# Kernel optimization log

Hardware: AMD Instinct MI355X
Metric: run time of the kernel (lower is better)

## Reference

```python
import jax, jax.numpy as jnp
import numpy as np

BN_EPS = 1e-5
L2_EPS = 1e-12


def setup_inputs() -> dict:
    key = jax.random.key(0)
    ks = jax.random.split(key, 4)
    B, C, H, W = 16, 384, 56, 56
    x = jax.random.normal(ks[0], (B, C, H, W), dtype=jnp.float32)
    w_qkv = jax.random.normal(ks[1], (3 * C, C), dtype=jnp.float32) * (1.0 / np.sqrt(C))
    b_qkv = jnp.zeros((3 * C,), dtype=jnp.float32)
    w_proj = jax.random.normal(ks[2], (C, C), dtype=jnp.float32) * (1.0 / np.sqrt(C))
    b_proj = jnp.zeros((C,), dtype=jnp.float32)
    bn_gamma = jnp.ones((C,), dtype=jnp.float32)
    bn_beta = jnp.zeros((C,), dtype=jnp.float32)
    bn_mean = jnp.zeros((C,), dtype=jnp.float32)
    bn_var = jnp.ones((C,), dtype=jnp.float32)
    temperature = jnp.ones((1,), dtype=jnp.float32)
    return {"x": x, "w_qkv": w_qkv, "b_qkv": b_qkv, "w_proj": w_proj,
            "b_proj": b_proj, "bn_gamma": bn_gamma, "bn_beta": bn_beta,
            "bn_mean": bn_mean, "bn_var": bn_var, "temperature": temperature}


def _l2norm_lastdim(t):
    # F.normalize(t, dim=-1): divide by max(||t||_2, eps)
    n = jnp.sqrt(jnp.sum(t * t, axis=-1, keepdims=True))
    return t / jnp.maximum(n, L2_EPS)


def reference(x, w_qkv, b_qkv, w_proj, b_proj, bn_gamma, bn_beta, bn_mean, bn_var, temperature):
    B, C, H, W = x.shape
    N = H * W
    # BatchNorm2d (eval mode, running stats)
    scale = bn_gamma / jnp.sqrt(bn_var + BN_EPS)          # [C]
    shift = bn_beta - bn_mean * scale                     # [C]
    xn = x * scale[None, :, None, None] + shift[None, :, None, None]
    # 1x1 conv qkv: C -> 3C, operate on flattened spatial [B, C, N]
    xn_f = xn.reshape(B, C, N)
    qkv = jnp.einsum('oc,bcn->bon', w_qkv, xn_f) + b_qkv[None, :, None]  # [B,3C,N]
    q, k, v = qkv[:, :C], qkv[:, C:2 * C], qkv[:, 2 * C:]
    q = _l2norm_lastdim(q)                                # [B,C,N]
    k = _l2norm_lastdim(k)
    # channel-transposed attention: [B,C,C]
    logits = jnp.einsum('bcn,bdn->bcd', q, k) * temperature[0]
    attn = jax.nn.softmax(logits, axis=-1)
    fused = jnp.einsum('bcd,bdn->bcn', attn, v)           # [B,C,N]
    # 1x1 proj conv + residual
    out = jnp.einsum('oc,bcn->bon', w_proj, fused) + b_proj[None, :, None]
    return x + out.reshape(B, C, H, W)
```

## Files before the change

kernel.cpp:

```cpp
#include <hip/hip_runtime.h>

#define BATCH 16
#define CCH   384
#define NSP   3136
#define OQKV  1152

typedef unsigned short u16;
typedef float  f32x4  __attribute__((ext_vector_type(4)));
typedef __bf16 bf16x8 __attribute__((ext_vector_type(8)));

__device__ __forceinline__ float bf2f(u16 u) {
  union { unsigned int i; float f; } v; v.i = ((unsigned int)u) << 16; return v.f;
}
__device__ __forceinline__ u16 f2bf(float f) {
  union { float f; unsigned int i; } v; v.f = f;
  unsigned int i = v.i;
  return (u16)((i + 0x7fffu + ((i >> 16) & 1u)) >> 16);
}
__device__ __forceinline__ float rdf(const void* p, long i, bool bf) {
  return bf ? bf2f(((const u16*)p)[i]) : ((const float*)p)[i];
}

__device__ __forceinline__ void gload_lds16(const u16* g, u16* l) {
  __builtin_amdgcn_global_load_lds(
      (const __attribute__((address_space(1))) void*)g,
      (__attribute__((address_space(3))) void*)l, 16, 0, 0);
}

__global__ void transpose_kernel(const void* __restrict__ x, u16* __restrict__ xt,
                                 const u16* __restrict__ probe) {
  const bool bf = (probe[0] == 0x3F80u);
  __shared__ float Ls[32 * 65];
  const int t = threadIdx.x;
  const int n0 = blockIdx.x * 64, c0 = blockIdx.y * 32, b = blockIdx.z;
  {
    const int c_l = t >> 3, n8 = (t & 7) * 8;
    const long src = ((long)b * CCH + c0 + c_l) * NSP + n0 + n8;
    float v[8];
    if (bf) {
      union { uint4 q; u16 e[8]; } u; u.q = *(const uint4*)((const u16*)x + src);
      #pragma unroll
      for (int i = 0; i < 8; i++) v[i] = bf2f(u.e[i]);
    } else {
      float4 a = *(const float4*)((const float*)x + src);
      float4 c = *(const float4*)((const float*)x + src + 4);
      v[0]=a.x; v[1]=a.y; v[2]=a.z; v[3]=a.w; v[4]=c.x; v[5]=c.y; v[6]=c.z; v[7]=c.w;
    }
    #pragma unroll
    for (int i = 0; i < 8; i++) Ls[c_l * 65 + n8 + i] = v[i];
  }
  __syncthreads();
  {
    const int n_l = t >> 2, c8 = (t & 3) * 8;
    union { uint4 q; u16 e[8]; } o;
    #pragma unroll
    for (int i = 0; i < 8; i++) o.e[i] = f2bf(Ls[(c8 + i) * 65 + n_l]);
    *(uint4*)(xt + ((long)b * NSP + n0 + n_l) * CCH + c0 + c8) = o.q;
  }
}

__global__ void prep_kernel(const void* __restrict__ w_qkv, const void* __restrict__ b_qkv,
                            const void* __restrict__ gamma, const void* __restrict__ beta,
                            const void* __restrict__ mean,  const void* __restrict__ var,
                            const void* __restrict__ b_proj, const void* __restrict__ w_proj,
                            u16* __restrict__ w_eff, float* __restrict__ b_eff,
                            float* __restrict__ bproj_f, u16* __restrict__ wp_bf,
                            const u16* __restrict__ probe) {
  const bool bf = (probe[0] == 0x3F80u);
  __shared__ float s_scale[CCH], s_shift[CCH];
  const int tid = threadIdx.x;
  for (int c = tid; c < CCH; c += 128) {
    float g = rdf(gamma, c, bf), bt = rdf(beta, c, bf);
    float mn = rdf(mean, c, bf), vr = rdf(var, c, bf);
    float sc = g * rsqrtf(vr + 1e-5f);
    s_scale[c] = sc; s_shift[c] = bt - mn * sc;
  }
  __syncthreads();
  const int o = blockIdx.x;
  float part = 0.f;
  for (int c = tid; c < CCH; c += 128) {
    float w = rdf(w_qkv, (long)o * CCH + c, bf);
    w_eff[o * CCH + c] = f2bf(w * s_scale[c]);
    part += w * s_shift[c];
  }
  for (int off = 32; off > 0; off >>= 1) part += __shfl_down(part, off, 64);
  __shared__ float s_part[2];
  if ((tid & 63) == 0) s_part[tid >> 6] = part;
  __syncthreads();
  if (tid == 0) b_eff[o] = rdf(b_qkv, o, bf) + s_part[0] + s_part[1];
  if (o < CCH) {
    for (int c = tid; c < CCH; c += 128)
      wp_bf[o * CCH + c] = f2bf(rdf(w_proj, (long)o * CCH + c, bf));
  }
  if (o == 0) {
    for (int c = tid; c < CCH; c += 128) bproj_f[c] = rdf(b_proj, c, bf);
  }
}

__global__ void zero_kernel(float4* __restrict__ p, long n4) {
  for (long i = (long)blockIdx.x * blockDim.x + threadIdx.x; i < n4;
       i += (long)gridDim.x * blockDim.x)
    p[i] = make_float4(0.f, 0.f, 0.f, 0.f);
}

template<int BM, int BN, int WGM, int WGN, int OUTM, bool BIASM, bool BIASN, bool RES, int KS>
__launch_bounds__(256)
__global__ void gemm_nt(const u16* __restrict__ A, const u16* __restrict__ B,
                        void* __restrict__ Cv,
                        const float* __restrict__ biasm, const float* __restrict__ biasn,
                        const void* __restrict__ resv,
                        int K, int lda, int ldb, int ldc,
                        long sA, long sB, long sC, long sRes, int zb,
                        const u16* __restrict__ probe) {
  constexpr int WM = BM / WGM, WN = BN / WGN;
  constexpr int FM = WM / 16,  FN = WN / 16;
  constexpr int NA = BM / 32,  NB = BN / 32;
  const bool f32io = (probe[0] != 0x3F80u);
  __shared__ __align__(16) u16 As[BM * 64];
  __shared__ __align__(16) u16 Bs[BN * 64];
  const int tid = threadIdx.x, wave = tid >> 6, lane = tid & 63;
  const int quad = lane >> 4, l16 = lane & 15;
  const int wm = wave / WGN, wn = wave % WGN;
  int z = blockIdx.z, kc = 0;
  if (KS > 1) { kc = z % KS; z /= KS; }
  A += z * sA; B += z * sB;
  const long cOff = (long)(zb + z) * sC;
  const long rOff = (long)(zb + z) * sRes;
  const int m0 = blockIdx.x * BM, n0 = blockIdx.y * BN;
  const int kLen = K / KS, kBeg = kc * kLen;

  const u16* ag[NA]; u16* al[NA];
  const u16* bg[NB]; u16* bl[NB];
  #pragma unroll
  for (int p = 0; p < NA; p++) {
    int u = tid + p * 256, r = u >> 3, k8 = u & 7;
    ag[p] = A + (long)(m0 + r) * lda + kBeg + ((k8 ^ (r & 7)) << 3);
    al[p] = &As[(wave * 64 + p * 256) * 8];
  }
  #pragma unroll
  for (int p = 0; p < NB; p++) {
    int u = tid + p * 256, r = u >> 3, k8 = u & 7;
    bg[p] = B + (long)(n0 + r) * ldb + kBeg + ((k8 ^ (r & 7)) << 3);
    bl[p] = &Bs[(wave * 64 + p * 256) * 8];
  }

  f32x4 acc[FM][FN] = {};

  for (int ks = 0; ks < kLen; ks += 64) {
    #pragma unroll
    for (int p = 0; p < NA; p++) { gload_lds16(ag[p], al[p]); ag[p] += 64; }
    #pragma unroll
    for (int p = 0; p < NB; p++) { gload_lds16(bg[p], bl[p]); bg[p] += 64; }
    __syncthreads();

    #pragma unroll
    for (int t = 0; t < 2; t++) {
      bf16x8 af[FM], bfr[FN];
      #pragma unroll
      for (int f = 0; f < FM; f++) {
        int r = wm * WM + f * 16 + l16;
        af[f] = *(const bf16x8*)&As[r * 64 + (((t * 4 + quad) ^ (l16 & 7)) << 3)];
      }
      #pragma unroll
      for (int g = 0; g < FN; g++) {
        int r = wn * WN + g * 16 + l16;
        bfr[g] = *(const bf16x8*)&Bs[r * 64 + (((t * 4 + quad) ^ (l16 & 7)) << 3)];
      }
      #pragma unroll
      for (int f = 0; f < FM; f++)
        #pragma unroll
        for (int g = 0; g < FN; g++)
          acc[f][g] = __builtin_amdgcn_mfma_f32_16x16x32_bf16(af[f], bfr[g], acc[f][g], 0, 0, 0);
    }
    __syncthreads();
  }

  #pragma unroll
  for (int f = 0; f < FM; f++) {
    #pragma unroll
    for (int g = 0; g < FN; g++) {
      #pragma unroll
      for (int reg = 0; reg < 4; reg++) {
        int mm = m0 + wm * WM + f * 16 + quad * 4 + reg;
        int nn = n0 + wn * WN + g * 16 + l16;
        float v = acc[f][g][reg];
        if (BIASM) v += biasm[mm];
        if (BIASN) v += biasn[nn];
        long off = (long)mm * ldc + nn;
        if (RES) {
          long ro = rOff + off;
          v += f32io ? ((const float*)resv)[ro] : bf2f(((const u16*)resv)[ro]);
        }
        if (OUTM == 1)      ((float*)Cv)[cOff + off] = v;
        else if (OUTM == 2) { if (f32io) ((float*)Cv)[cOff + off] = v;
                              else       ((u16*)Cv)[cOff + off]   = f2bf(v); }
        else if (OUTM == 3) atomicAdd((float*)Cv + cOff + off, v);
        else                ((u16*)Cv)[cOff + off] = f2bf(v);
      }
    }
  }
}

__global__ void norms_kernel(const u16* __restrict__ qk, float* __restrict__ invn) {
  const int row = blockIdx.x, b = blockIdx.y;
  const u16* p = qk + (long)b * 768 * NSP + (long)row * NSP;
  float s = 0.f;
  for (int i = threadIdx.x * 8; i < NSP; i += 256 * 8) {
    union { uint4 v; u16 u[8]; } x; x.v = *(const uint4*)(p + i);
    #pragma unroll
    for (int j = 0; j < 8; j++) { float t = bf2f(x.u[j]); s += t * t; }
  }
  for (int off = 32; off > 0; off >>= 1) s += __shfl_down(s, off, 64);
  __shared__ float sp[4];
  if ((threadIdx.x & 63) == 0) sp[threadIdx.x >> 6] = s;
  __syncthreads();
  if (threadIdx.x == 0) {
    float t = sp[0] + sp[1] + sp[2] + sp[3];
    invn[b * 768 + row] = 1.f / fmaxf(sqrtf(t), 1e-12f);
  }
}

__global__ void softmax_kernel(const float* __restrict__ logits, const float* __restrict__ invn,
                               const void* __restrict__ temp, u16* __restrict__ attn,
                               const u16* __restrict__ probe) {
  const bool bfm = (probe[0] == 0x3F80u);
  const int c = blockIdx.x, b = blockIdx.y;
  const float* row = logits + ((long)b * CCH + c) * CCH;
  const float rq = invn[b * 768 + c];
  const float T = rdf(temp, 0, bfm);
  const int tid = threadIdx.x;
  float v[3]; float mx = -1e30f;
  #pragma unroll
  for (int j = 0; j < 3; j++) {
    int d = tid + j * 128;
    float xv = row[d] * rq * invn[b * 768 + 384 + d] * T;
    v[j] = xv; mx = fmaxf(mx, xv);
  }
  for (int off = 32; off > 0; off >>= 1) mx = fmaxf(mx, __shfl_down(mx, off, 64));
  __shared__ float sm[2];
  if ((tid & 63) == 0) sm[tid >> 6] = mx;
  __syncthreads();
  mx = fmaxf(sm[0], sm[1]);
  float s = 0.f;
  #pragma unroll
  for (int j = 0; j < 3; j++) { v[j] = __expf(v[j] - mx); s += v[j]; }
  for (int off = 32; off > 0; off >>= 1) s += __shfl_down(s, off, 64);
  __shared__ float ss[2];
  if ((tid & 63) == 0) ss[tid >> 6] = s;
  __syncthreads();
  s = ss[0] + ss[1];
  const float inv = 1.f / s;
  u16* arow = attn + ((long)b * CCH + c) * CCH;
  #pragma unroll
  for (int j = 0; j < 3; j++) arow[tid + j * 128] = f2bf(v[j] * inv);
}

extern "C" void kernel_launch(void* const* d_in, const int* in_sizes, int n_in,
                              void* d_out, int out_size, void* d_ws, size_t ws_size,
                              hipStream_t stream) {
  const void* x      = d_in[0];
  const void* w_qkv  = d_in[1];
  const void* b_qkv  = d_in[2];
  const void* w_proj = d_in[3];
  const void* b_proj = d_in[4];
  const void* gamma  = d_in[5];
  const void* beta   = d_in[6];
  const void* mean   = d_in[7];
  const void* var    = d_in[8];
  const void* temp   = d_in[9];
  const u16* probe = (const u16*)gamma;

  const size_t SZ_XT    = (size_t)BATCH * NSP * CCH * 2;
  const size_t SZ_WEFF  = (size_t)OQKV * CCH * 2;
  const size_t SZ_WPBF  = (size_t)CCH * CCH * 2;
  const size_t SZ_BEFF  = (size_t)OQKV * 4;
  const size_t SZ_BPROJ = (size_t)CCH * 4;
  const size_t SZ_INVN  = (size_t)BATCH * 768 * 4;
  const size_t SZ_QK_B  = (size_t)768 * NSP * 2;
  const size_t SZ_VT_B  = (size_t)NSP * CCH * 2;
  const size_t SZ_FT_B  = (size_t)NSP * CCH * 2;
  const size_t SZ_LOG_B = (size_t)CCH * CCH * 4;
  const size_t SZ_ATT_B = (size_t)CCH * CCH * 2;
  const size_t P = SZ_QK_B + SZ_VT_B + SZ_FT_B + SZ_LOG_B + SZ_ATT_B;
  const size_t FIXED = SZ_XT + SZ_WEFF + SZ_WPBF + SZ_BEFF + SZ_BPROJ + SZ_INVN;

  long chunk = 1;
  if (ws_size >= FIXED + P) {
    chunk = (long)((ws_size - FIXED) / P);
    if (chunk > BATCH) chunk = BATCH;
    if (chunk < 1) chunk = 1;
  }

  char* ws = (char*)d_ws;
  u16*   xt      = (u16*)ws;   ws += SZ_XT;
  u16*   w_eff   = (u16*)ws;   ws += SZ_WEFF;
  u16*   wp_bf   = (u16*)ws;   ws += SZ_WPBF;
  float* b_eff   = (float*)ws; ws += SZ_BEFF;
  float* bproj_f = (float*)ws; ws += SZ_BPROJ;
  float* invn    = (float*)ws; ws += SZ_INVN;
  float* logits  = (float*)ws; ws += SZ_LOG_B * chunk;
  u16*   attn    = (u16*)ws;   ws += SZ_ATT_B * chunk;
  u16*   qk      = (u16*)ws;   ws += SZ_QK_B * chunk;
  u16*   v_t     = (u16*)ws;   ws += SZ_VT_B * chunk;
  u16*   fused_t = (u16*)ws;   ws += SZ_FT_B * chunk;

  transpose_kernel<<<dim3(NSP / 64, CCH / 32, BATCH), dim3(256), 0, stream>>>(x, xt, probe);
  prep_kernel<<<dim3(OQKV), dim3(128), 0, stream>>>(
      w_qkv, b_qkv, gamma, beta, mean, var, b_proj, w_proj,
      w_eff, b_eff, bproj_f, wp_bf, probe);

  const long sX  = (long)CCH * NSP;
  const long sXT = (long)NSP * CCH;
  const long sQK = (long)768 * NSP;
  const long sVT = (long)NSP * CCH;
  const long sFT = (long)NSP * CCH;
  const long sLG = (long)CCH * CCH;
  const long sAT = (long)CCH * CCH;

  for (long b0 = 0; b0 < BATCH; b0 += chunk) {
    const int nb = (int)((BATCH - b0) < chunk ? (BATCH - b0) : chunk);
    const u16* xtb = xt + b0 * sXT;

    gemm_nt<256, 64, 4, 1, 0, true, false, false, 1>
        <<<dim3(3, 49, nb), dim3(256), 0, stream>>>(
        w_eff, xtb, qk, b_eff, nullptr, nullptr,
        CCH, CCH, CCH, NSP, 0L, sXT, sQK, 0L, 0, probe);

    gemm_nt<64, 192, 2, 2, 0, false, true, false, 1>
        <<<dim3(49, 2, nb), dim3(256), 0, stream>>>(
        xtb, w_eff + (long)768 * CCH, v_t, nullptr, b_eff + 768, nullptr,
        CCH, CCH, CCH, CCH, sXT, 0L, sVT, 0L, 0, probe);

    norms_kernel<<<dim3(768, nb), dim3(256), 0, stream>>>(qk, invn + b0 * 768);

    zero_kernel<<<dim3(512), dim3(256), 0, stream>>>(
        (float4*)logits, (long)nb * sLG / 4);

    gemm_nt<96, 96, 2, 2, 3, false, false, false, 7>
        <<<dim3(4, 4, nb * 7), dim3(256), 0, stream>>>(
        qk, qk + (long)CCH * NSP, logits, nullptr, nullptr, nullptr,
        NSP, NSP, NSP, CCH, sQK, sQK, sLG, 0L, 0, probe);

    softmax_kernel<<<dim3(CCH, nb), dim3(128), 0, stream>>>(
        logits, invn + b0 * 768, temp, attn, probe);

    gemm_nt<64, 192, 2, 2, 0, false, false, false, 1>
        <<<dim3(49, 2, nb), dim3(256), 0, stream>>>(
        v_t, attn, fused_t, nullptr, nullptr, nullptr,
        CCH, CCH, CCH, CCH, sVT, sAT, sFT, 0L, 0, probe);

    gemm_nt<192, 64, 2, 2, 2, true, false, true, 1>
        <<<dim3(2, 49, nb), dim3(256), 0, stream>>>(
        wp_bf, fused_t, d_out, bproj_f, nullptr, x,
        CCH, CCH, CCH, NSP, 0L, sFT, sX, sX, (int)b0, probe);
  }
}
```

Measured before the change: 461.0 us.

## Double-buffer GEMM LDS, fuse QK norms into epilogue, replace split-K atomics

The GEMM main loop now double-buffers its LDS tiles so the next k-tile's global-to-LDS loads are issued while the current tile is computed. The QK projection epilogue accumulates per-row sums of squares with shuffles and atomics, which removes the separate norms kernel. Split-K logits are written to separate partial buffers and reduced inside softmax instead of using a zero-fill plus atomicAdd, and several tile shapes and grids are retuned. The cost is twice the LDS per block, which may lower occupancy, seven times more logits workspace that may force smaller batch chunks, and norms computed from fp32 values before bf16 rounding.

```diff
diff --git a/kernel.cpp b/kernel.cpp
--- a/kernel.cpp
+++ b/kernel.cpp
@@ -4,6 +4,7 @@
 #define CCH   384
 #define NSP   3136
 #define OQKV  1152
+#define KSPL  7
 
 typedef unsigned short u16;
 typedef float  f32x4  __attribute__((ext_vector_type(4)));
@@ -103,7 +104,8 @@
     p[i] = make_float4(0.f, 0.f, 0.f, 0.f);
 }
 
-template<int BM, int BN, int WGM, int WGN, int OUTM, bool BIASM, bool BIASN, bool RES, int KS>
+template<int BM, int BN, int WGM, int WGN, int OUTM, bool BIASM, bool BIASN, bool RES,
+         int KS, bool QKN>
 __launch_bounds__(256)
 __global__ void gemm_nt(const u16* __restrict__ A, const u16* __restrict__ B,
                         void* __restrict__ Cv,
@@ -111,13 +113,16 @@
                         const void* __restrict__ resv,
                         int K, int lda, int ldb, int ldc,
                         long sA, long sB, long sC, long sRes, int zb,
+                        float* __restrict__ qns,
                         const u16* __restrict__ probe) {
   constexpr int WM = BM / WGM, WN = BN / WGN;
   constexpr int FM = WM / 16,  FN = WN / 16;
   constexpr int NA = BM / 32,  NB = BN / 32;
   const bool f32io = (probe[0] != 0x3F80u);
-  __shared__ __align__(16) u16 As[BM * 64];
-  __shared__ __align__(16) u16 Bs[BN * 64];
+  __shared__ __align__(16) u16 As0[BM * 64];
+  __shared__ __align__(16) u16 As1[BM * 64];
+  __shared__ __align__(16) u16 Bs0[BN * 64];
+  __shared__ __align__(16) u16 Bs1[BN * 64];
   const int tid = threadIdx.x, wave = tid >> 6, lane = tid & 63;
   const int quad = lane >> 4, l16 = lane & 15;
   const int wm = wave / WGN, wn = wave % WGN;
@@ -129,42 +134,40 @@
   const int m0 = blockIdx.x * BM, n0 = blockIdx.y * BN;
   const int kLen = K / KS, kBeg = kc * kLen;
 
-  const u16* ag[NA]; u16* al[NA];
-  const u16* bg[NB]; u16* bl[NB];
+  const u16* ag[NA];
+  const u16* bg[NB];
   #pragma unroll
   for (int p = 0; p < NA; p++) {
     int u = tid + p * 256, r = u >> 3, k8 = u & 7;
     ag[p] = A + (long)(m0 + r) * lda + kBeg + ((k8 ^ (r & 7)) << 3);
-    al[p] = &As[(wave * 64 + p * 256) * 8];
   }
   #pragma unroll
   for (int p = 0; p < NB; p++) {
     int u = tid + p * 256, r = u >> 3, k8 = u & 7;
     bg[p] = B + (long)(n0 + r) * ldb + kBeg + ((k8 ^ (r & 7)) << 3);
-    bl[p] = &Bs[(wave * 64 + p * 256) * 8];
   }
 
   f32x4 acc[FM][FN] = {};
 
-  for (int ks = 0; ks < kLen; ks += 64) {
-    #pragma unroll
-    for (int p = 0; p < NA; p++) { gload_lds16(ag[p], al[p]); ag[p] += 64; }
-    #pragma unroll
-    for (int p = 0; p < NB; p++) { gload_lds16(bg[p], bl[p]); bg[p] += 64; }
-    __syncthreads();
-
+  auto stage = [&](u16* dA, u16* dB) {
+    #pragma unroll
+    for (int p = 0; p < NA; p++) { gload_lds16(ag[p], dA + (p * 256 + wave * 64) * 8); ag[p] += 64; }
+    #pragma unroll
+    for (int p = 0; p < NB; p++) { gload_lds16(bg[p], dB + (p * 256 + wave * 64) * 8); bg[p] += 64; }
+  };
+  auto compute = [&](const u16* sAp, const u16* sBp) {
     #pragma unroll
     for (int t = 0; t < 2; t++) {
       bf16x8 af[FM], bfr[FN];
       #pragma unroll
       for (int f = 0; f < FM; f++) {
         int r = wm * WM + f * 16 + l16;
-        af[f] = *(const bf16x8*)&As[r * 64 + (((t * 4 + quad) ^ (l16 & 7)) << 3)];
+        af[f] = *(const bf16x8*)&sAp[r * 64 + (((t * 4 + quad) ^ (l16 & 7)) << 3)];
       }
       #pragma unroll
       for (int g = 0; g < FN; g++) {
         int r = wn * WN + g * 16 + l16;
-        bfr[g] = *(const bf16x8*)&Bs[r * 64 + (((t * 4 + quad) ^ (l16 & 7)) << 3)];
+        bfr[g] = *(const bf16x8*)&sBp[r * 64 + (((t * 4 + quad) ^ (l16 & 7)) << 3)];
       }
       #pragma unroll
       for (int f = 0; f < FM; f++)
@@ -172,16 +175,31 @@
         for (int g = 0; g < FN; g++)
           acc[f][g] = __builtin_amdgcn_mfma_f32_16x16x32_bf16(af[f], bfr[g], acc[f][g], 0, 0, 0);
     }
+  };
+
+  const int nt = kLen >> 6;
+  stage(As0, Bs0);
+  __syncthreads();
+  int t = 0;
+  while (true) {
+    if (t + 1 < nt) stage(As1, Bs1);
+    compute(As0, Bs0);
+    if (++t >= nt) break;
     __syncthreads();
+    if (t + 1 < nt) stage(As0, Bs0);
+    compute(As1, Bs1);
+    if (++t >= nt) break;
+    __syncthreads();
   }
 
   #pragma unroll
   for (int f = 0; f < FM; f++) {
     #pragma unroll
-    for (int g = 0; g < FN; g++) {
-      #pragma unroll
-      for (int reg = 0; reg < 4; reg++) {
-        int mm = m0 + wm * WM + f * 16 + quad * 4 + reg;
+    for (int reg = 0; reg < 4; reg++) {
+      const int mm = m0 + wm * WM + f * 16 + quad * 4 + reg;
+      float s2 = 0.f;
+      #pragma unroll
+      for (int g = 0; g < FN; g++) {
         int nn = n0 + wn * WN + g * 16 + l16;
         float v = acc[f][g][reg];
         if (BIASM) v += biasm[mm];
@@ -191,49 +209,46 @@
           long ro = rOff + off;
           v += f32io ? ((const float*)resv)[ro] : bf2f(((const u16*)resv)[ro]);
         }
-        if (OUTM == 1)      ((float*)Cv)[cOff + off] = v;
-        else if (OUTM == 2) { if (f32io) ((float*)Cv)[cOff + off] = v;
-                              else       ((u16*)Cv)[cOff + off]   = f2bf(v); }
-        else if (OUTM == 3) atomicAdd((float*)Cv + cOff + off, v);
-        else                ((u16*)Cv)[cOff + off] = f2bf(v);
+        if (OUTM == 1) {
+          long po = cOff + off + ((KS > 1) ? (long)kc * sRes : 0L);
+          ((float*)Cv)[po] = v;
+        } else if (OUTM == 2) {
+          if (f32io) ((float*)Cv)[cOff + off] = v;
+          else       ((u16*)Cv)[cOff + off]   = f2bf(v);
+        } else {
+          ((u16*)Cv)[cOff + off] = f2bf(v);
+        }
+        if (QKN) s2 += v * v;
+      }
+      if (QKN) {
+        s2 += __shfl_xor(s2, 1, 16);
+        s2 += __shfl_xor(s2, 2, 16);
+        s2 += __shfl_xor(s2, 4, 16);
+        s2 += __shfl_xor(s2, 8, 16);
+        if (l16 == 0) atomicAdd(qns + (long)(zb + z) * 768 + mm, s2);
       }
     }
   }
 }
 
-__global__ void norms_kernel(const u16* __restrict__ qk, float* __restrict__ invn) {
-  const int row = blockIdx.x, b = blockIdx.y;
-  const u16* p = qk + (long)b * 768 * NSP + (long)row * NSP;
-  float s = 0.f;
-  for (int i = threadIdx.x * 8; i < NSP; i += 256 * 8) {
-    union { uint4 v; u16 u[8]; } x; x.v = *(const uint4*)(p + i);
-    #pragma unroll
-    for (int j = 0; j < 8; j++) { float t = bf2f(x.u[j]); s += t * t; }
-  }
-  for (int off = 32; off > 0; off >>= 1) s += __shfl_down(s, off, 64);
-  __shared__ float sp[4];
-  if ((threadIdx.x & 63) == 0) sp[threadIdx.x >> 6] = s;
-  __syncthreads();
-  if (threadIdx.x == 0) {
-    float t = sp[0] + sp[1] + sp[2] + sp[3];
-    invn[b * 768 + row] = 1.f / fmaxf(sqrtf(t), 1e-12f);
-  }
-}
-
-__global__ void softmax_kernel(const float* __restrict__ logits, const float* __restrict__ invn,
+__global__ void softmax_kernel(const float* __restrict__ logits, const float* __restrict__ sums,
                                const void* __restrict__ temp, u16* __restrict__ attn,
-                               const u16* __restrict__ probe) {
+                               int zb, const u16* __restrict__ probe) {
   const bool bfm = (probe[0] == 0x3F80u);
   const int c = blockIdx.x, b = blockIdx.y;
-  const float* row = logits + ((long)b * CCH + c) * CCH;
-  const float rq = invn[b * 768 + c];
+  const long base = ((long)b * KSPL) * (CCH * CCH) + (long)c * CCH;
+  const float rq = 1.f / fmaxf(sqrtf(sums[(zb + b) * 768 + c]), 1e-12f);
   const float T = rdf(temp, 0, bfm);
   const int tid = threadIdx.x;
   float v[3]; float mx = -1e30f;
   #pragma unroll
   for (int j = 0; j < 3; j++) {
     int d = tid + j * 128;
-    float xv = row[d] * rq * invn[b * 768 + 384 + d] * T;
+    float lv = 0.f;
+    #pragma unroll
+    for (int kc = 0; kc < KSPL; kc++) lv += logits[base + (long)kc * CCH * CCH + d];
+    float rd = 1.f / fmaxf(sqrtf(sums[(zb + b) * 768 + 384 + d]), 1e-12f);
+    float xv = lv * rq * rd * T;
     v[j] = xv; mx = fmaxf(mx, xv);
   }
   for (int off = 32; off > 0; off >>= 1) mx = fmaxf(mx, __shfl_down(mx, off, 64));
@@ -275,14 +290,14 @@
   const size_t SZ_WPBF  = (size_t)CCH * CCH * 2;
   const size_t SZ_BEFF  = (size_t)OQKV * 4;
   const size_t SZ_BPROJ = (size_t)CCH * 4;
-  const size_t SZ_INVN  = (size_t)BATCH * 768 * 4;
+  const size_t SZ_SUMS  = (size_t)BATCH * 768 * 4;
   const size_t SZ_QK_B  = (size_t)768 * NSP * 2;
   const size_t SZ_VT_B  = (size_t)NSP * CCH * 2;
   const size_t SZ_FT_B  = (size_t)NSP * CCH * 2;
-  const size_t SZ_LOG_B = (size_t)CCH * CCH * 4;
+  const size_t SZ_LOG_B = (size_t)KSPL * CCH * CCH * 4;
   const size_t SZ_ATT_B = (size_t)CCH * CCH * 2;
   const size_t P = SZ_QK_B + SZ_VT_B + SZ_FT_B + SZ_LOG_B + SZ_ATT_B;
-  const size_t FIXED = SZ_XT + SZ_WEFF + SZ_WPBF + SZ_BEFF + SZ_BPROJ + SZ_INVN;
+  const size_t FIXED = SZ_XT + SZ_WEFF + SZ_WPBF + SZ_BEFF + SZ_BPROJ + SZ_SUMS;
 
   long chunk = 1;
   if (ws_size >= FIXED + P) {
@@ -297,7 +312,7 @@
   u16*   wp_bf   = (u16*)ws;   ws += SZ_WPBF;
   float* b_eff   = (float*)ws; ws += SZ_BEFF;
   float* bproj_f = (float*)ws; ws += SZ_BPROJ;
-  float* invn    = (float*)ws; ws += SZ_INVN;
+  float* sums    = (float*)ws; ws += SZ_SUMS;
   float* logits  = (float*)ws; ws += SZ_LOG_B * chunk;
   u16*   attn    = (u16*)ws;   ws += SZ_ATT_B * chunk;
   u16*   qk      = (u16*)ws;   ws += SZ_QK_B * chunk;
@@ -308,50 +323,46 @@
   prep_kernel<<<dim3(OQKV), dim3(128), 0, stream>>>(
       w_qkv, b_qkv, gamma, beta, mean, var, b_proj, w_proj,
       w_eff, b_eff, bproj_f, wp_bf, probe);
+  zero_kernel<<<dim3(12), dim3(256), 0, stream>>>((float4*)sums, (long)BATCH * 768 / 4);
 
   const long sX  = (long)CCH * NSP;
   const long sXT = (long)NSP * CCH;
   const long sQK = (long)768 * NSP;
   const long sVT = (long)NSP * CCH;
   const long sFT = (long)NSP * CCH;
-  const long sLG = (long)CCH * CCH;
+  const long sLG = (long)KSPL * CCH * CCH;
   const long sAT = (long)CCH * CCH;
 
   for (long b0 = 0; b0 < BATCH; b0 += chunk) {
     const int nb = (int)((BATCH - b0) < chunk ? (BATCH - b0) : chunk);
     const u16* xtb = xt + b0 * sXT;
 
-    gemm_nt<256, 64, 4, 1, 0, true, false, false, 1>
+    gemm_nt<128, 64, 2, 2, 0, true, false, false, 1, true>
+        <<<dim3(6, 49, nb), dim3(256), 0, stream>>>(
+        w_eff, xtb, qk, b_eff, nullptr, nullptr,
+        CCH, CCH, CCH, NSP, 0L, sXT, sQK, 0L, (int)b0, sums, probe);
+
+    gemm_nt<64, 128, 1, 4, 0, false, true, false, 1, false>
+        <<<dim3(49, 3, nb), dim3(256), 0, stream>>>(
+        xtb, w_eff + (long)768 * CCH, v_t, nullptr, b_eff + 768, nullptr,
+        CCH, CCH, CCH, CCH, sXT, 0L, sVT, 0L, 0, nullptr, probe);
+
+    gemm_nt<96, 96, 2, 2, 1, false, false, false, KSPL, false>
+        <<<dim3(4, 4, nb * KSPL), dim3(256), 0, stream>>>(
+        qk, qk + (long)CCH * NSP, logits, nullptr, nullptr, nullptr,
+        NSP, NSP, NSP, CCH, sQK, sQK, sLG, (long)CCH * CCH, 0, nullptr, probe);
+
+    softmax_kernel<<<dim3(CCH, nb), dim3(128), 0, stream>>>(
+        logits, sums, temp, attn, (int)b0, probe);
+
+    gemm_nt<64, 128, 1, 4, 0, false, false, false, 1, false>
+        <<<dim3(49, 3, nb), dim3(256), 0, stream>>>(
+        v_t, attn, fused_t, nullptr, nullptr, nullptr,
+        CCH, CCH, CCH, CCH, sVT, sAT, sFT, 0L, 0, nullptr, probe);
+
+    gemm_nt<128, 64, 2, 2, 2, true, false, true, 1, false>
         <<<dim3(3, 49, nb), dim3(256), 0, stream>>>(
-        w_eff, xtb, qk, b_eff, nullptr, nullptr,
-        CCH, CCH, CCH, NSP, 0L, sXT, sQK, 0L, 0, probe);
-
-    gemm_nt<64, 192, 2, 2, 0, false, true, false, 1>
-        <<<dim3(49, 2, nb), dim3(256), 0, stream>>>(
-        xtb, w_eff + (long)768 * CCH, v_t, nullptr, b_eff + 768, nullptr,
-        CCH, CCH, CCH, CCH, sXT, 0L, sVT, 0L, 0, probe);
-
-    norms_kernel<<<dim3(768, nb), dim3(256), 0, stream>>>(qk, invn + b0 * 768);
-
-    zero_kernel<<<dim3(512), dim3(256), 0, stream>>>(
-        (float4*)logits, (long)nb * sLG / 4);
-
-    gemm_nt<96, 96, 2, 2, 3, false, false, false, 7>
-        <<<dim3(4, 4, nb * 7), dim3(256), 0, stream>>>(
-        qk, qk + (long)CCH * NSP, logits, nullptr, nullptr, nullptr,
-        NSP, NSP, NSP, CCH, sQK, sQK, sLG, 0L, 0, probe);
-
-    softmax_kernel<<<dim3(CCH, nb), dim3(128), 0, stream>>>(
-        logits, invn + b0 * 768, temp, attn, probe);
-
-    gemm_nt<64, 192, 2, 2, 0, false, false, false, 1>
-        <<<dim3(49, 2, nb), dim3(256), 0, stream>>>(
-        v_t, attn, fused_t, nullptr, nullptr, nullptr,
-        CCH, CCH, CCH, CCH, sVT, sAT, sFT, 0L, 0, probe);
-
-    gemm_nt<192, 64, 2, 2, 2, true, false, true, 1>
-        <<<dim3(2, 49, nb), dim3(256), 0, stream>>>(
         wp_bf, fused_t, d_out, bproj_f, nullptr, x,
-        CCH, CCH, CCH, NSP, 0L, sFT, sX, sX, (int)b0, probe);
-  }
-}
+        CCH, CCH, CCH, NSP, 0L, sFT, sX, sX, (int)b0, nullptr, probe);
+  }
+}
```

Measured after the change: 466.5 us. No clear change (+1.2%).
